# Performance work log

Measured on AMD Instinct MI355X. Metric: run time of the kernel, lower is better.

Reference implementation:

```python
import jax, jax.numpy as jnp
import numpy as np

SCALES = (1, 2, 4)
KS = 5          # conv kernel size
POOL = 2        # maxpool kernel & stride


def coarse_grain(x, s):
    # non-overlapping mean pool along last axis
    B, C, L = x.shape
    Lc = L // s
    return x[:, :, : Lc * s].reshape(B, C, Lc, s).mean(axis=-1)


def conv1d(x, w, b):
    # x: [B, C_in, L], w: [C_out, C_in, K] (torch layout), VALID padding, stride 1
    y = jax.lax.conv_general_dilated(
        x, w, window_strides=(1,), padding='VALID',
        dimension_numbers=('NCH', 'OIH', 'NCH'))
    return y + b[None, :, None]


def maxpool1d(x, k):
    B, C, L = x.shape
    Lp = L // k
    return x[:, :, : Lp * k].reshape(B, C, Lp, k).max(axis=-1)


def conv_block(x, w1, b1, w2, b2):
    x = maxpool1d(jax.nn.relu(conv1d(x, w1, b1)), POOL)
    x = maxpool1d(jax.nn.relu(conv1d(x, w2, b2)), POOL)
    return x


def setup_inputs() -> dict:
    key = jax.random.key(0)
    ks = jax.random.split(key, 9)
    B, C, NWL = 2048, 4, 480
    C1, C2 = 16, 32
    # flatten size per model's own arithmetic: sum over scales of conv/pool output lens * C2
    F = (117 + 57 + 27) * C2  # 6432
    NOUT = 5
    sc = lambda fan_in: 1.0 / np.sqrt(fan_in)
    return {
        'x':  jax.random.normal(ks[0], (B, C, NWL), dtype=jnp.float32),
        'w1': jax.random.uniform(ks[1], (C1, C, KS), jnp.float32, -sc(C * KS), sc(C * KS)),
        'b1': jax.random.uniform(ks[2], (C1,), jnp.float32, -sc(C * KS), sc(C * KS)),
        'w2': jax.random.uniform(ks[3], (C2, C1, KS), jnp.float32, -sc(C1 * KS), sc(C1 * KS)),
        'b2': jax.random.uniform(ks[4], (C2,), jnp.float32, -sc(C1 * KS), sc(C1 * KS)),
        'wl': jax.random.uniform(ks[5], (F, F), jnp.float32, -sc(F), sc(F)),
        'bl': jax.random.uniform(ks[6], (F,), jnp.float32, -sc(F), sc(F)),
        'wo': jax.random.uniform(ks[7], (NOUT, F), jnp.float32, -sc(F), sc(F)),
        'bo': jax.random.uniform(ks[8], (NOUT,), jnp.float32, -sc(F), sc(F)),
    }


def reference(x, w1, b1, w2, b2, wl, bl, wo, bo):
    # multi-scale feature mapping: shared ConvBlock applied to each coarse-grained scale
    feats = [conv_block(coarse_grain(x, s), w1, b1, w2, b2) for s in SCALES]
    f = jnp.concatenate(feats, axis=-1)            # [B, 32, 201]
    f = f.reshape(f.shape[0], -1)                  # [B, 6432]
    # the SAME linear layer (shared weights) is applied 4 times in torch
    for _ in range(4):
        f = jax.nn.relu(f @ wl.T + bl)
    return f @ wo.T + bo                           # [B, 5]
```

## Files before the change

kernel.cpp:

```cpp
#include <hip/hip_runtime.h>

typedef _Float16 v8h __attribute__((ext_vector_type(8)));
typedef _Float16 v4h __attribute__((ext_vector_type(4)));
typedef float    v4f __attribute__((ext_vector_type(4)));

#define GK 6432
#define GN 6432
#define GM 2048
#define GNPAD 6528

__global__ void convert_w(const float* __restrict__ wl, _Float16* __restrict__ Wh)
{
    const int row = blockIdx.y;
    const int col = (blockIdx.x * 256 + threadIdx.x) * 4;
    if (col >= GK) return;
    v4h h;
    if (row < GN) {
        const float4 f = *(const float4*)(wl + (long)row * GK + col);
        h[0] = (_Float16)f.x; h[1] = (_Float16)f.y;
        h[2] = (_Float16)f.z; h[3] = (_Float16)f.w;
    } else {
        h[0] = (_Float16)0.f; h[1] = (_Float16)0.f;
        h[2] = (_Float16)0.f; h[3] = (_Float16)0.f;
    }
    *(v4h*)(Wh + (long)row * GK + col) = h;
}

#define SX   0
#define SX2  2048
#define SX4  3136
#define SW1  3712
#define SB1  4032
#define SW2  4048
#define SB2  6608
#define SP1  6640
#define LDSZ 13808

__global__ __launch_bounds__(256) void conv_feat(
    const float* __restrict__ x,
    const float* __restrict__ w1, const float* __restrict__ b1,
    const float* __restrict__ w2, const float* __restrict__ b2,
    _Float16* __restrict__ F0)
{
    __shared__ float lds[LDSZ];
    const int tid = threadIdx.x;
    const long b  = blockIdx.x;

    for (int i = tid; i < 1920; i += 256) {
        int c = i / 480, t = i % 480;
        lds[SX + c * 512 + t] = x[(b * 4 + c) * 480 + t];
    }
    for (int i = tid; i < 320;  i += 256) lds[SW1 + i] = w1[i];
    for (int i = tid; i < 16;   i += 256) lds[SB1 + i] = b1[i];
    for (int i = tid; i < 2560; i += 256) lds[SW2 + i] = w2[i];
    for (int i = tid; i < 32;   i += 256) lds[SB2 + i] = b2[i];
    __syncthreads();

    for (int i = tid; i < 960; i += 256) {
        int c = i / 240, t = i % 240;
        lds[SX2 + c * 272 + t] = 0.5f * (lds[SX + c * 512 + 2 * t] + lds[SX + c * 512 + 2 * t + 1]);
    }
    for (int i = tid; i < 480; i += 256) {
        int c = i / 120, t = i % 120;
        float s = lds[SX + c * 512 + 4 * t]     + lds[SX + c * 512 + 4 * t + 1]
                + lds[SX + c * 512 + 4 * t + 2] + lds[SX + c * 512 + 4 * t + 3];
        lds[SX4 + c * 144 + t] = 0.25f * s;
    }
    __syncthreads();

    for (int jid = tid; jid < 16 * 34; jid += 256) {
        const int c1 = jid / 34, rid = jid % 34;
        const int sidx = (rid < 19) ? 0 : (rid < 29 ? 1 : 2);
        const int r0   = (sidx == 0) ? rid : (sidx == 1 ? rid - 19 : rid - 29);
        const int u0   = r0 * 13;
        const int xbase  = (sidx == 0) ? SX  : (sidx == 1 ? SX2 : SX4);
        const int xpitch = (sidx == 0) ? 512 : (sidx == 1 ? 272 : 144);
        const int P      = (sidx == 0) ? 238 : (sidx == 1 ? 118 : 58);
        const int pofs   = (sidx == 0) ? 0   : (sidx == 1 ? 238 : 356);

        float acc[26];
        const float bias = lds[SB1 + c1];
        #pragma unroll
        for (int i = 0; i < 26; ++i) acc[i] = bias;

        #pragma unroll
        for (int ci = 0; ci < 4; ++ci) {
            float w[30];
            const float* xr = &lds[xbase + ci * xpitch + 2 * u0];
            #pragma unroll
            for (int q = 0; q < 15; ++q) {
                float2 t2 = *(const float2*)(xr + 2 * q);
                w[2 * q] = t2.x; w[2 * q + 1] = t2.y;
            }
            float wt[5];
            #pragma unroll
            for (int k = 0; k < 5; ++k) wt[k] = lds[SW1 + (c1 * 4 + ci) * 5 + k];
            #pragma unroll
            for (int i = 0; i < 26; ++i) {
                #pragma unroll
                for (int k = 0; k < 5; ++k) acc[i] += w[i + k] * wt[k];
            }
        }
        #pragma unroll
        for (int i = 0; i < 13; ++i) {
            int u = u0 + i;
            if (u < P)
                lds[SP1 + c1 * 448 + pofs + u] = fmaxf(fmaxf(acc[2 * i], acc[2 * i + 1]), 0.f);
        }
    }
    __syncthreads();

    for (int jid = tid; jid < 32 * 17; jid += 256) {
        const int c2 = jid / 17, rid = jid % 17;
        const int sidx = (rid < 9) ? 0 : (rid < 14 ? 1 : 2);
        const int r0   = (sidx == 0) ? rid : (sidx == 1 ? rid - 9 : rid - 14);
        const int v0   = r0 * 13;
        const int pbase = (sidx == 0) ? 0   : (sidx == 1 ? 238 : 356);
        const int Pv    = (sidx == 0) ? 117 : (sidx == 1 ? 57  : 27);
        const int vout  = (sidx == 0) ? 0   : (sidx == 1 ? 117 : 174);

        float acc[26];
        const float bias = lds[SB2 + c2];
        #pragma unroll
        for (int i = 0; i < 26; ++i) acc[i] = bias;

        for (int c1 = 0; c1 < 16; ++c1) {
            float w[30];
            const float* pr = &lds[SP1 + c1 * 448 + pbase + 2 * v0];
            #pragma unroll
            for (int q = 0; q < 15; ++q) {
                float2 t2 = *(const float2*)(pr + 2 * q);
                w[2 * q] = t2.x; w[2 * q + 1] = t2.y;
            }
            float wt[5];
            #pragma unroll
            for (int k = 0; k < 5; ++k) wt[k] = lds[SW2 + (c2 * 16 + c1) * 5 + k];
            #pragma unroll
            for (int i = 0; i < 26; ++i) {
                #pragma unroll
                for (int k = 0; k < 5; ++k) acc[i] += w[i + k] * wt[k];
            }
        }
        #pragma unroll
        for (int i = 0; i < 13; ++i) {
            int v = v0 + i;
            if (v < Pv) {
                float f = fmaxf(fmaxf(acc[2 * i], acc[2 * i + 1]), 0.f);
                F0[b * GK + c2 * 201 + vout + v] = (_Float16)f;
            }
        }
    }
}

__global__ __launch_bounds__(128, 2) void gemm_relu(
    const _Float16* __restrict__ A, const _Float16* __restrict__ Bw,
    const float* __restrict__ bias, _Float16* __restrict__ C)
{
    __shared__ _Float16 sA[2][128 * 32];
    __shared__ _Float16 sB[2][128 * 32];
    const int tid  = threadIdx.x;
    const int lane = tid & 63;
    const int wave = tid >> 6;

    const int id = blockIdx.x;
    int n_t, m_t;
    if (id < 768) {
        n_t = ((id >> 7) << 3) | (id & 7);
        m_t = (id >> 3) & 15;
    } else {
        const int r = id - 768;
        n_t = 48 + r % 3;
        m_t = r / 3;
    }
    const long tile_m = (long)m_t * 128;
    const long tile_n = (long)n_t * 128;

    const int lr   = lane >> 2;
    const int sfn  = (lr & 3) ^ ((lr >> 2) & 3);
    const int scol = (((lane & 3) ^ sfn) << 3);
    const _Float16* gS = (wave == 0)
        ? A  + (tile_m + lr) * (long)GK + scol
        : Bw + (tile_n + lr) * (long)GK + scol;

    const int fr = lane & 15;
    const int fp = lane >> 4;
    const int fslot = fp ^ ((fr & 3) ^ ((fr >> 2) & 3));
    int aoff[8], boff[4];
    #pragma unroll
    for (int i = 0; i < 8; ++i)
        aoff[i] = ((i << 4) + fr) * 32 + (fslot << 3);
    #pragma unroll
    for (int j = 0; j < 4; ++j)
        boff[j] = ((wave << 6) + (j << 4) + fr) * 32 + (fslot << 3);

    v4f acc[8][4];
    #pragma unroll
    for (int i = 0; i < 8; ++i) {
        #pragma unroll
        for (int j = 0; j < 4; ++j) { v4f z = {0.f, 0.f, 0.f, 0.f}; acc[i][j] = z; }
    }

    auto stage = [&](int k0, int buf) {
        _Float16* dst = (wave == 0) ? sA[buf] : sB[buf];
        #pragma unroll
        for (int t = 0; t < 8; ++t) {
            __builtin_amdgcn_global_load_lds(
                (const __attribute__((address_space(1))) void*)(gS + (t * 16) * (long)GK + k0),
                (__attribute__((address_space(3))) void*)(dst + t * 16 * 32), 16, 0, 0);
        }
    };

    stage(0, 0);
    int pb = 0;
    for (int k0 = 0; k0 < GK; k0 += 32) {
        __syncthreads();
        if (k0 + 32 < GK) stage(k0 + 32, pb ^ 1);

        const _Float16* cA = sA[pb];
        const _Float16* cB = sB[pb];
        v8h af[8], bf[4];
        #pragma unroll
        for (int j = 0; j < 4; ++j) bf[j] = *(const v8h*)&cB[boff[j]];
        #pragma unroll
        for (int i = 0; i < 8; ++i) af[i] = *(const v8h*)&cA[aoff[i]];
        #pragma unroll
        for (int i = 0; i < 8; ++i) {
            #pragma unroll
            for (int j = 0; j < 4; ++j)
                acc[i][j] = __builtin_amdgcn_mfma_f32_16x16x32_f16(af[i], bf[j], acc[i][j], 0, 0, 0);
        }
        pb ^= 1;
    }

    #pragma unroll
    for (int j = 0; j < 4; ++j) {
        const long col = tile_n + (wave << 6) + (j << 4) + fr;
        if (col < GN) {
            const float bv = bias[col];
            #pragma unroll
            for (int i = 0; i < 8; ++i) {
                const long row = tile_m + (i << 4) + (fp << 2);
                #pragma unroll
                for (int r = 0; r < 4; ++r) {
                    float v = acc[i][j][r] + bv;
                    v = v > 0.f ? v : 0.f;
                    C[(row + r) * (long)GN + col] = (_Float16)v;
                }
            }
        }
    }
}

__global__ __launch_bounds__(256) void final_out(
    const _Float16* __restrict__ F, const float* __restrict__ wo,
    const float* __restrict__ bo, float* __restrict__ out)
{
    __shared__ float red[4][8];
    const long b   = blockIdx.x;
    const int tid  = threadIdx.x;
    const int lane = tid & 63;
    const int wave = tid >> 6;
    float acc[5] = {0.f, 0.f, 0.f, 0.f, 0.f};
    const _Float16* f = F + b * GK;

    const int c1 = (wave + 1) * 402;
    for (int c = wave * 402 + lane; c < c1; c += 64) {
        const int k = c << 2;
        v4h f4 = *(const v4h*)(f + k);
        const float f0 = (float)f4[0], f1 = (float)f4[1];
        const float f2 = (float)f4[2], f3 = (float)f4[3];
        #pragma unroll
        for (int o = 0; o < 5; ++o) {
            const float4 w4 = *(const float4*)(wo + o * GK + k);
            acc[o] += f0 * w4.x + f1 * w4.y + f2 * w4.z + f3 * w4.w;
        }
    }
    #pragma unroll
    for (int o = 0; o < 5; ++o) {
        #pragma unroll
        for (int off = 32; off > 0; off >>= 1) acc[o] += __shfl_down(acc[o], off, 64);
    }
    if (lane == 0) {
        #pragma unroll
        for (int o = 0; o < 5; ++o) red[wave][o] = acc[o];
    }
    __syncthreads();
    if (tid < 5)
        out[b * 5 + tid] = red[0][tid] + red[1][tid] + red[2][tid] + red[3][tid] + bo[tid];
}

extern "C" void kernel_launch(void* const* d_in, const int* in_sizes, int n_in,
                              void* d_out, int out_size, void* d_ws, size_t ws_size,
                              hipStream_t stream)
{
    const float* x  = (const float*)d_in[0];
    const float* w1 = (const float*)d_in[1];
    const float* b1 = (const float*)d_in[2];
    const float* w2 = (const float*)d_in[3];
    const float* b2 = (const float*)d_in[4];
    const float* wl = (const float*)d_in[5];
    const float* bl = (const float*)d_in[6];
    const float* wo = (const float*)d_in[7];
    const float* bo = (const float*)d_in[8];
    float* out = (float*)d_out;

    char* ws = (char*)d_ws;
    _Float16* Wh = (_Float16*)ws;
    _Float16* F0 = (_Float16*)(ws + 83976192);
    _Float16* F1 = (_Float16*)(ws + 83976192 + 26345472);

    convert_w<<<dim3(7, GNPAD), 256, 0, stream>>>(wl, Wh);
    conv_feat<<<GM, 256, 0, stream>>>(x, w1, b1, w2, b2, F0);
    gemm_relu<<<816, 128, 0, stream>>>(F0, Wh, bl, F1);
    gemm_relu<<<816, 128, 0, stream>>>(F1, Wh, bl, F0);
    gemm_relu<<<816, 128, 0, stream>>>(F0, Wh, bl, F1);
    gemm_relu<<<816, 128, 0, stream>>>(F1, Wh, bl, F0);
    final_out<<<GM, 256, 0, stream>>>(F0, wo, bo, out);
}
```

Measured before the change: 1.348 ms.

## Load GEMM MFMA fragments directly from global memory into double-buffered registers

The fp16 GEMM no longer stages A and B tiles through LDS with async global-to-LDS copies and block barriers. Each wave now reads its MFMA operand fragments straight from global memory into two register buffer sets, alternating loads and MFMAs. The wave split also changes: each wave now covers 64 rows by all 128 columns instead of 128 rows by 64 columns. This removes LDS traffic and __syncthreads, but both waves now fetch the same B rows, and the per-lane row-strided 16-byte loads coalesce poorly. That leans heavily on cache and adds register pressure.

```diff
diff --git a/kernel.cpp b/kernel.cpp
--- a/kernel.cpp
+++ b/kernel.cpp
@@ -156,8 +156,6 @@
     const _Float16* __restrict__ A, const _Float16* __restrict__ Bw,
     const float* __restrict__ bias, _Float16* __restrict__ C)
 {
-    __shared__ _Float16 sA[2][128 * 32];
-    __shared__ _Float16 sB[2][128 * 32];
     const int tid  = threadIdx.x;
     const int lane = tid & 63;
     const int wave = tid >> 6;
@@ -175,71 +173,55 @@
     const long tile_m = (long)m_t * 128;
     const long tile_n = (long)n_t * 128;
 
-    const int lr   = lane >> 2;
-    const int sfn  = (lr & 3) ^ ((lr >> 2) & 3);
-    const int scol = (((lane & 3) ^ sfn) << 3);
-    const _Float16* gS = (wave == 0)
-        ? A  + (tile_m + lr) * (long)GK + scol
-        : Bw + (tile_n + lr) * (long)GK + scol;
-
     const int fr = lane & 15;
     const int fp = lane >> 4;
-    const int fslot = fp ^ ((fr & 3) ^ ((fr >> 2) & 3));
-    int aoff[8], boff[4];
+    const _Float16* pA = A  + (tile_m + (wave << 6) + fr) * (long)GK + (fp << 3);
+    const _Float16* pB = Bw + (tile_n + fr) * (long)GK + (fp << 3);
+
+    v4f acc[4][8];
     #pragma unroll
-    for (int i = 0; i < 8; ++i)
-        aoff[i] = ((i << 4) + fr) * 32 + (fslot << 3);
+    for (int i = 0; i < 4; ++i) {
+        #pragma unroll
+        for (int j = 0; j < 8; ++j) { v4f z = {0.f, 0.f, 0.f, 0.f}; acc[i][j] = z; }
+    }
+
+    v8h a0[4], b0[8], a1[4], b1[8];
+
+    auto loadf = [&](v8h* a, v8h* b, int k) {
+        #pragma unroll
+        for (int i = 0; i < 4; ++i)
+            a[i] = *(const v8h*)(pA + (long)(i << 4) * GK + k);
+        #pragma unroll
+        for (int j = 0; j < 8; ++j)
+            b[j] = *(const v8h*)(pB + (long)(j << 4) * GK + k);
+    };
+    auto domfma = [&](v8h* a, v8h* b) {
+        #pragma unroll
+        for (int i = 0; i < 4; ++i) {
+            #pragma unroll
+            for (int j = 0; j < 8; ++j)
+                acc[i][j] = __builtin_amdgcn_mfma_f32_16x16x32_f16(a[i], b[j], acc[i][j], 0, 0, 0);
+        }
+    };
+
+    loadf(a0, b0, 0);
+    for (int it = 0; it < 100; ++it) {
+        const int kb = it << 6;
+        loadf(a1, b1, kb + 32);
+        domfma(a0, b0);
+        loadf(a0, b0, kb + 64);
+        domfma(a1, b1);
+    }
+    domfma(a0, b0);
+
     #pragma unroll
-    for (int j = 0; j < 4; ++j)
-        boff[j] = ((wave << 6) + (j << 4) + fr) * 32 + (fslot << 3);
-
-    v4f acc[8][4];
-    #pragma unroll
-    for (int i = 0; i < 8; ++i) {
-        #pragma unroll
-        for (int j = 0; j < 4; ++j) { v4f z = {0.f, 0.f, 0.f, 0.f}; acc[i][j] = z; }
-    }
-
-    auto stage = [&](int k0, int buf) {
-        _Float16* dst = (wave == 0) ? sA[buf] : sB[buf];
-        #pragma unroll
-        for (int t = 0; t < 8; ++t) {
-            __builtin_amdgcn_global_load_lds(
-                (const __attribute__((address_space(1))) void*)(gS + (t * 16) * (long)GK + k0),
-                (__attribute__((address_space(3))) void*)(dst + t * 16 * 32), 16, 0, 0);
-        }
-    };
-
-    stage(0, 0);
-    int pb = 0;
-    for (int k0 = 0; k0 < GK; k0 += 32) {
-        __syncthreads();
-        if (k0 + 32 < GK) stage(k0 + 32, pb ^ 1);
-
-        const _Float16* cA = sA[pb];
-        const _Float16* cB = sB[pb];
-        v8h af[8], bf[4];
-        #pragma unroll
-        for (int j = 0; j < 4; ++j) bf[j] = *(const v8h*)&cB[boff[j]];
-        #pragma unroll
-        for (int i = 0; i < 8; ++i) af[i] = *(const v8h*)&cA[aoff[i]];
-        #pragma unroll
-        for (int i = 0; i < 8; ++i) {
-            #pragma unroll
-            for (int j = 0; j < 4; ++j)
-                acc[i][j] = __builtin_amdgcn_mfma_f32_16x16x32_f16(af[i], bf[j], acc[i][j], 0, 0, 0);
-        }
-        pb ^= 1;
-    }
-
-    #pragma unroll
-    for (int j = 0; j < 4; ++j) {
-        const long col = tile_n + (wave << 6) + (j << 4) + fr;
+    for (int j = 0; j < 8; ++j) {
+        const long col = tile_n + (j << 4) + fr;
         if (col < GN) {
             const float bv = bias[col];
             #pragma unroll
-            for (int i = 0; i < 8; ++i) {
-                const long row = tile_m + (i << 4) + (fp << 2);
+            for (int i = 0; i < 4; ++i) {
+                const long row = tile_m + (wave << 6) + (i << 4) + (fp << 2);
                 #pragma unroll
                 for (int r = 0; r < 4; ++r) {
                     float v = acc[i][j][r] + bv;
```

Result: slower. 1.963 ms (+45.6%).
